# Optimization experiments

Measured on AMD Instinct MI355X. Metric: run time of the kernel, lower is better.

The kernel has to match this reference:

```python
import jax, jax.numpy as jnp
import numpy as np

B, L, V, E = 8, 2000, 50000, 300      # batch, doc len, vocab, embed dim
NL, LW = 8922, 10                     # num labels, words per label desc
F_, K, H = 200, 10, 200               # num_filters, kernel_size, label_hidden
FEAT = E + H                          # feat_size = 500


def setup_inputs():
    key = jax.random.key(0)
    ks = jax.random.split(key, 12)
    n = lambda k, sh, s=0.02: jax.random.normal(k, sh, jnp.float32) * s
    x = jax.random.randint(ks[0], (B, L), 0, V)
    y = (jax.random.uniform(ks[1], (B, NL)) < 0.01).astype(jnp.float32)
    mask = jnp.ones((B, L), jnp.float32)
    word_emb = n(ks[2], (V, E), 0.1)
    label_idx_matrix = jax.random.randint(ks[3], (NL, LW), 0, V)
    label_idx_mask = jnp.ones((NL, LW), jnp.float32)
    adj_matrix = (jax.random.uniform(ks[4], (NL, NL)) < 0.002).astype(jnp.float32)
    num_neighbors = jnp.maximum(adj_matrix.sum(axis=1), 1.0)
    return {
        'x': x, 'y': y, 'mask': mask,
        'word_emb': word_emb,
        'label_idx_matrix': label_idx_matrix,
        'label_idx_mask': label_idx_mask,
        'adj_matrix': adj_matrix,
        'num_neighbors': num_neighbors,
        'Wg': n(ks[5], (E, H)), 'bg': jnp.zeros((H,), jnp.float32),
        'Wc': n(ks[6], (F_, E, K)), 'bc': jnp.zeros((F_,), jnp.float32),
        'Wp': n(ks[7], (F_, E)), 'bp': jnp.zeros((E,), jnp.float32),
        'Wo': n(ks[8], (F_, FEAT)), 'bo': jnp.zeros((FEAT,), jnp.float32),
    }


def reference(x, y, mask, word_emb, label_idx_matrix, label_idx_mask,
              adj_matrix, num_neighbors, Wg, bg, Wc, bc, Wp, bp, Wo, bo):
    # --- average label embedding over label description words ---
    le = word_emb[label_idx_matrix]                              # [NL, LW, E]
    avg = (le * label_idx_mask[..., None]).sum(1)
    avg = avg / label_idx_mask.sum(axis=-1, keepdims=True)       # [NL, E]
    # --- conv graph encoder over label hierarchy ---
    agg = (adj_matrix @ avg) / num_neighbors[:, None]            # [NL, E]
    gh = jax.nn.relu(agg @ Wg + bg)                              # [NL, H]
    graph_emb = jnp.concatenate([avg, gh], axis=-1)              # [NL, FEAT]
    # --- document encoding (dropouts are identity in eval) ---
    xe = word_emb[x] * mask[..., None]                           # [B, L, E]
    c = jax.lax.conv_general_dilated(
        xe.transpose(0, 2, 1), Wc, window_strides=(1,), padding='VALID',
        dimension_numbers=('NCH', 'OIH', 'NCH')) + bc[None, :, None]
    c = jax.nn.relu(c).transpose(0, 2, 1)                        # [B, Lp, F]
    pj = jnp.tanh(c @ Wp + bp)                                   # [B, Lp, E]
    # --- label-wise attention ---
    scores = jnp.einsum('ble,ne->bnl', pj, avg)                  # [B, NL, Lp]
    attn = jax.nn.softmax(scores, axis=-1)
    attn_out = jnp.einsum('bnl,blf->bnf', attn, c)               # [B, NL, F]
    proj = jax.nn.relu(attn_out @ Wo + bo)                       # [B, NL, FEAT]
    logits = (graph_emb[None] * proj).sum(-1)                    # [B, NL]
    # --- BCE-with-logits (sum) / batch ---
    bce = jnp.maximum(logits, 0.0) - logits * y + jnp.log1p(jnp.exp(-jnp.abs(logits)))
    loss = bce.sum() / B
    return (logits, loss)
```

## Files before the change

kernel.cpp:

```cpp
#include <hip/hip_runtime.h>
#include <math.h>

#define B_    8
#define L_    2000
#define V_    50000
#define E_    300
#define NL_   8922
#define NLP_  8960
#define LW_   10
#define F_    200
#define KW_   10
#define H_    200
#define FEAT_ 500
#define LP_   1991

typedef __attribute__((ext_vector_type(8))) short bf16x8;
typedef __attribute__((ext_vector_type(4))) float f32x4;

static __device__ __forceinline__ unsigned short f2b(float f) {
  unsigned u = __builtin_bit_cast(unsigned, f);
  u += 0x7FFF + ((u >> 16) & 1);
  return (unsigned short)(u >> 16);
}
static __device__ __forceinline__ float b2f(unsigned short u) {
  unsigned v = ((unsigned)u) << 16;
  return __builtin_bit_cast(float, v);
}
static __device__ __forceinline__ float fast_tanh(float x) {
  x = fminf(fmaxf(x, -10.f), 10.f);
  float t = __expf(2.f * x);
  return (t - 1.f) / (t + 1.f);
}
static __device__ __forceinline__ void stage16(const void* g, void* l) {
  __builtin_amdgcn_global_load_lds(
      (const __attribute__((address_space(1))) unsigned int*)g,
      (__attribute__((address_space(3))) unsigned int*)l, 16, 0, 0);
}

#define MFMA(a, b, c) __builtin_amdgcn_mfma_f32_16x16x32_bf16(a, b, c, 0, 0, 0)


__global__ __launch_bounds__(256) void k_avg(const float* __restrict__ we,
                                             const int* __restrict__ lidx,
                                             const float* __restrict__ lmask,
                                             float* __restrict__ avg,
                                             unsigned short* __restrict__ avgb,
                                             unsigned short* __restrict__ geF) {
  int idx = blockIdx.x * 256 + threadIdx.x;
  if (idx >= NLP_ * 80) return;
  int n = idx / 80, e4 = idx - n * 80;
  if (n >= NL_ || e4 >= 75) {
    *(ushort4*)&avgb[(size_t)n * 320 + e4 * 4] = make_ushort4(0, 0, 0, 0);
    return;
  }
  float ax = 0.f, ay = 0.f, az = 0.f, aw = 0.f, ms = 0.f;
#pragma unroll
  for (int w = 0; w < LW_; ++w) {
    float mw = lmask[n * LW_ + w];
    const float4 f = *(const float4*)&we[(size_t)lidx[n * LW_ + w] * E_ + e4 * 4];
    ax = fmaf(f.x, mw, ax); ay = fmaf(f.y, mw, ay);
    az = fmaf(f.z, mw, az); aw = fmaf(f.w, mw, aw);
    ms += mw;
  }
  float inv = 1.f / ms;
  float4 v = {ax * inv, ay * inv, az * inv, aw * inv};
  *(float4*)&avg[(size_t)n * 300 + e4 * 4] = v;
  *(ushort4*)&avgb[(size_t)n * 320 + e4 * 4] =
      make_ushort4(f2b(v.x), f2b(v.y), f2b(v.z), f2b(v.w));
  int ntg = n >> 4, quad = (n >> 2) & 3, r = n & 3;
  int ftg = (e4 * 4) >> 4, c0 = (e4 * 4) & 15;
  size_t tb = (((size_t)ntg * 32 + ftg) << 8);
  float vv[4] = {v.x, v.y, v.z, v.w};
#pragma unroll
  for (int t = 0; t < 4; ++t)
    geF[(tb + quad * 16 + c0 + t) * 4 + r] = f2b(vv[t]);
}

__global__ __launch_bounds__(256) void k_agg(const float* __restrict__ adj,
                                             const float* __restrict__ avg,
                                             const float* __restrict__ nnb,
                                             unsigned short* __restrict__ aggF) {
  __shared__ int s_idx[1024];
  __shared__ float s_val[1024];
  __shared__ float s_agg[320];
  __shared__ int s_cnt;
  const int n = blockIdx.x;
  const int tid = threadIdx.x;
  if (tid == 0) s_cnt = 0;
  __syncthreads();
  const float* row = adj + (size_t)n * NL_;
  for (int j = tid; j < NL_; j += 256) {
    float v = row[j];
    if (v != 0.f) {
      int p = atomicAdd(&s_cnt, 1);
      if (p < 1024) { s_idx[p] = j; s_val[p] = v; }
    }
  }
  __syncthreads();
  const int m = min(s_cnt, 1024);
  const float inv = 1.f / nnb[n];
  float a0 = 0.f, a1 = 0.f;
  for (int i = 0; i < m; ++i) {
    const float* ar = avg + (size_t)s_idx[i] * 300;
    float v = s_val[i];
    a0 = fmaf(v, ar[tid], a0);
    if (tid < E_ - 256) a1 = fmaf(v, ar[tid + 256], a1);
  }
  s_agg[tid] = a0 * inv;
  if (tid < E_ - 256) s_agg[tid + 256] = a1 * inv;
  if (tid >= 44 && tid < 64) s_agg[tid + 256] = 0.f;
  __syncthreads();
  if (tid < 320) {
    int e = tid;
    int ks = e >> 5, qA = (e >> 3) & 3, jj = e & 7;
    aggF[(((size_t)((n >> 4) * 10 + ks)) << 9) + ((qA << 4) + (n & 15)) * 8 + jj] =
        f2b(s_agg[e]);
  }
}

__global__ __launch_bounds__(256) void k_gh2(const unsigned short* __restrict__ aggF,
                                             const unsigned short* __restrict__ WgF,
                                             const float* __restrict__ bg,
                                             unsigned short* __restrict__ geF) {
  const int n0g = blockIdx.x * 64;
  const int tid = threadIdx.x;
  const int wv = tid >> 6, lane = tid & 63, quad = lane >> 4, c16 = lane & 15;
  const int mt = wv;
  f32x4 acc[14];
#pragma unroll
  for (int nt = 0; nt < 14; ++nt) acc[nt] = (f32x4){0.f, 0.f, 0.f, 0.f};
#pragma unroll
  for (int ks = 0; ks < 10; ++ks) {
    bf16x8 a = *(const bf16x8*)
        &aggF[(((size_t)(((n0g >> 4) + mt) * 10 + ks)) << 9) + (lane << 3)];
#pragma unroll
    for (int nt = 0; nt < 14; ++nt) {
      bf16x8 bw = *(const bf16x8*)&WgF[(((size_t)(nt * 10 + ks)) << 9) + (lane << 3)];
      acc[nt] = MFMA(a, bw, acc[nt]);
    }
  }
#pragma unroll
  for (int nt = 0; nt < 14; ++nt) {
    int h = nt * 16 + c16;
    if (h < H_) {
      float bgv = bg[h];
      int feat = 300 + h;
      int ftg = feat >> 4, cg = feat & 15;
#pragma unroll
      for (int r = 0; r < 4; ++r) {
        int n = n0g + mt * 16 + quad * 4 + r;
        if (n < NL_)
          geF[((((size_t)(n >> 4) * 32 + ftg) << 8) + (quad << 4) + cg) * 4 + r] =
              f2b(fmaxf(acc[nt][r] + bgv, 0.f));
      }
    }
  }
}

__global__ __launch_bounds__(256) void k_wprep(const float* __restrict__ Wc,
                                               const float* __restrict__ Wp,
                                               const float* __restrict__ Wo,
                                               const float* __restrict__ Wg,
                                               unsigned short* __restrict__ WcF,
                                               unsigned short* __restrict__ WpF,
                                               unsigned short* __restrict__ WoF,
                                               unsigned short* __restrict__ WgF) {
  int idx = blockIdx.x * 256 + threadIdx.x;
  if (idx < 819200) {
    int koff = idx / (16 * 10 * 512);
    int rem = idx - koff * (16 * 10 * 512);
    int ft = rem / (10 * 512);
    int rem2 = rem - ft * (10 * 512);
    int ks = rem2 >> 9, t = rem2 & 511;
    int lane = t >> 3, j = t & 7;
    int f = ft * 16 + (lane & 15);
    int e = ks * 32 + (lane >> 4) * 8 + j;
    float v = (f < F_ && e < E_) ? Wc[((size_t)f * E_ + e) * KW_ + koff] : 0.f;
    WcF[idx] = f2b(v);
    return;
  }
  idx -= 819200;
  if (idx < 71680) {
    int et = idx / (7 * 512);
    int rem = idx - et * (7 * 512);
    int kt = rem >> 9, t = rem & 511;
    int lane = t >> 3, j = t & 7;
    int e = et * 16 + (lane & 15);
    int f = kt * 32 + (lane >> 4) * 8 + j;
    float v = (e < E_ && f < F_) ? Wp[(size_t)f * E_ + e] : 0.f;
    WpF[idx] = f2b(v);
    return;
  }
  idx -= 71680;
  if (idx < 114688) {
    int g = idx / (7 * 512);
    int rem = idx - g * (7 * 512);
    int kt = rem >> 9, t = rem & 511;
    int lane = t >> 3, j = t & 7;
    int feat = g * 16 + (lane & 15);
    int f = kt * 32 + (lane >> 4) * 8 + j;
    float v = (feat < FEAT_ && f < F_) ? Wo[(size_t)f * FEAT_ + feat] : 0.f;
    WoF[idx] = f2b(v);
    return;
  }
  idx -= 114688;
  if (idx < 71680) {
    int nt = idx / (10 * 512);
    int rem = idx - nt * (10 * 512);
    int ks = rem >> 9, t = rem & 511;
    int lane = t >> 3, j = t & 7;
    int h = nt * 16 + (lane & 15);
    int e = ks * 32 + (lane >> 4) * 8 + j;
    float v = (h < H_ && e < E_) ? Wg[(size_t)e * H_ + h] : 0.f;
    WgF[idx] = f2b(v);
  }
}

__global__ __launch_bounds__(256) void k_cpj(const int* __restrict__ x,
                                             const float* __restrict__ mask,
                                             const float* __restrict__ we,
                                             const unsigned short* __restrict__ WcF,
                                             const float* __restrict__ bc,
                                             const unsigned short* __restrict__ WpF,
                                             const float* __restrict__ bp,
                                             unsigned short* __restrict__ cF,
                                             unsigned short* __restrict__ pjF) {
  __shared__ __attribute__((aligned(16))) unsigned char smem[78896];
  unsigned short* s_xe  = (unsigned short*)smem;
  unsigned short* s_pjF = (unsigned short*)smem;
  unsigned short* s_cA  = (unsigned short*)(smem + 50224);

  const int b = blockIdx.y;
  const int l0 = blockIdx.x * 64;
  const int tid = threadIdx.x;
  const int wv = tid >> 6, lane = tid & 63, quad = lane >> 4, c16 = lane & 15;

  for (int i = tid; i < 73 * 75; i += 256) {
    int row = i / 75, e4 = i - row * 75;
    int l = l0 + row;
    float4 v = {0.f, 0.f, 0.f, 0.f};
    if (l < L_) {
      int bl = b * L_ + l;
      v = *(const float4*)&we[(size_t)x[bl] * E_ + e4 * 4];
      float mm = mask[bl];
      v.x *= mm; v.y *= mm; v.z *= mm; v.w *= mm;
    }
    *(ushort4*)&s_xe[row * 344 + e4 * 4] =
        make_ushort4(f2b(v.x), f2b(v.y), f2b(v.z), f2b(v.w));
  }
  for (int i = tid; i < 73 * 5; i += 256) {
    int row = i / 5, c = i - row * 5;
    *(ushort4*)&s_xe[row * 344 + (75 + c) * 4] = make_ushort4(0, 0, 0, 0);
  }
  __syncthreads();

  f32x4 acc[4][4];
#pragma unroll
  for (int mt = 0; mt < 4; ++mt)
#pragma unroll
    for (int j = 0; j < 4; ++j) acc[mt][j] = (f32x4){0.f, 0.f, 0.f, 0.f};
  for (int koff = 0; koff < KW_; ++koff) {
#pragma unroll
    for (int ks = 0; ks < 10; ++ks) {
      bf16x8 a[4];
#pragma unroll
      for (int mt = 0; mt < 4; ++mt)
        a[mt] = *(const bf16x8*)&s_xe[(mt * 16 + c16 + koff) * 344 + ks * 32 + quad * 8];
#pragma unroll
      for (int jj = 0; jj < 4; ++jj) {
        bf16x8 bw = *(const bf16x8*)
            &WcF[(((size_t)((koff * 16 + wv * 4 + jj) * 10 + ks)) << 9) + (lane << 3)];
#pragma unroll
        for (int mt = 0; mt < 4; ++mt) acc[mt][jj] = MFMA(a[mt], bw, acc[mt][jj]);
      }
    }
  }
  unsigned short* cFb = cF + (size_t)b * (16 * 64 * 512);
#pragma unroll
  for (int jj = 0; jj < 4; ++jj) {
    const int ft2 = wv * 4 + jj;
    const int f = ft2 * 16 + c16;
    const float bcv = (f < F_) ? bc[f] : 0.f;
    const int kt = ft2 >> 1;
    const int qA = ((ft2 & 1) << 1) | (c16 >> 3);
    const int jA = c16 & 7;
#pragma unroll
    for (int mt = 0; mt < 4; ++mt) {
      unsigned short u[4];
#pragma unroll
      for (int r = 0; r < 4; ++r) u[r] = f2b(fmaxf(acc[mt][jj][r] + bcv, 0.f));
      int su = (l0 >> 5) + (mt >> 1);
      int lane_c = ((((mt & 1) << 1) | (quad >> 1)) << 4) + c16;
      *(ushort4*)&cFb[(((size_t)(ft2 * 64 + su)) << 9) + lane_c * 8 + ((quad & 1) << 2)] =
          make_ushort4(u[0], u[1], u[2], u[3]);
      if (ft2 < 14) {
#pragma unroll
        for (int r = 0; r < 4; ++r)
          s_cA[(((size_t)(mt * 7 + kt)) << 9) + ((qA << 4) + quad * 4 + r) * 8 + jA] = u[r];
      }
    }
  }
  __syncthreads();

  f32x4 pacc[4][5];
#pragma unroll
  for (int mt = 0; mt < 4; ++mt)
#pragma unroll
    for (int j = 0; j < 5; ++j) pacc[mt][j] = (f32x4){0.f, 0.f, 0.f, 0.f};
#pragma unroll
  for (int kt = 0; kt < 7; ++kt) {
    bf16x8 a[4];
#pragma unroll
    for (int mt = 0; mt < 4; ++mt)
      a[mt] = *(const bf16x8*)&s_cA[(((size_t)(mt * 7 + kt)) << 9) + (lane << 3)];
#pragma unroll
    for (int j = 0; j < 5; ++j) {
      bf16x8 bw = *(const bf16x8*)
          &WpF[(((size_t)((wv * 5 + j) * 7 + kt)) << 9) + (lane << 3)];
#pragma unroll
      for (int mt = 0; mt < 4; ++mt) pacc[mt][j] = MFMA(a[mt], bw, pacc[mt][j]);
    }
  }
  __syncthreads();
#pragma unroll
  for (int j = 0; j < 5; ++j) {
    const int et = wv * 5 + j;
    const int e = et * 16 + c16;
    const float bpe = (e < E_) ? bp[e] : 0.f;
    const int ks = et >> 1;
    const int qP = ((et & 1) << 1) | (c16 >> 3);
    const int jP = c16 & 7;
#pragma unroll
    for (int mt = 0; mt < 4; ++mt) {
#pragma unroll
      for (int r = 0; r < 4; ++r) {
        float v = (e < E_) ? fast_tanh(pacc[mt][j][r] + bpe) : 0.f;
        s_pjF[(((size_t)(mt * 10 + ks)) << 9) + ((qP << 4) + quad * 4 + r) * 8 + jP] = f2b(v);
      }
    }
  }
  __syncthreads();
  {
    unsigned short* dst = pjF + (((size_t)((b * 128 + (l0 >> 4)) * 10)) << 9);
    for (int i = tid; i < 2560; i += 256)
      *(uint4*)&dst[i * 8] = *(const uint4*)&s_pjF[i * 8];
  }
}

__global__ __launch_bounds__(256, 2) void k_attn(
    const unsigned short* __restrict__ pjF,
    const unsigned short* __restrict__ cF,
    const unsigned short* __restrict__ avgb,
    const unsigned short* __restrict__ WoF,
    const unsigned short* __restrict__ geF,
    const float* __restrict__ bo,
    float* __restrict__ out) {
  __shared__ __attribute__((aligned(16))) unsigned char smem[74752];
  unsigned short* Ps  = (unsigned short*)(smem + 69632);
  float* s_wsum = (float*)(smem + 73728);
  float* s_sum  = (float*)(smem + 74240);
  float* s_lg   = (float*)(smem + 74496);
  unsigned short* AOs = (unsigned short*)smem;

  const int tid = threadIdx.x;
  const int b  = blockIdx.x & 7;
  const int n0 = (blockIdx.x >> 3) << 6;
  const int wv = tid >> 6, lane = tid & 63, quad = lane >> 4, c16 = lane & 15;
  const int lh = wv & 1, nh = wv >> 1;

  if (tid < 64) s_lg[tid] = 0.f;

  bf16x8 bavg[10][2];
#pragma unroll
  for (int ks = 0; ks < 10; ++ks)
#pragma unroll
    for (int nt = 0; nt < 2; ++nt)
      bavg[ks][nt] = *(const bf16x8*)
          &avgb[(size_t)(n0 + nh * 32 + nt * 16 + c16) * 320 + ks * 32 + quad * 8];

  const unsigned short* pjb = pjF + (size_t)b * (128 * 10 * 512);
  const unsigned short* cFb = cF + (size_t)b * (16 * 64 * 512);

  {
    const unsigned char* pg = (const unsigned char*)pjb;
#pragma unroll
    for (int t = 0; t < 5; ++t) {
      int off = (wv * 5 + t) << 10;
      stage16(pg + off + lane * 16, smem + off);
    }
#pragma unroll
    for (int t = 0; t < 4; ++t) {
      int ft = wv + t * 4;
      if (ft < 14)
        stage16((const unsigned char*)cFb + (((size_t)(ft * 64)) << 10) + lane * 16,
                smem + 20480 + (ft << 10));
    }
  }

  f32x4 o[2][7];
#pragma unroll
  for (int nt = 0; nt < 2; ++nt)
#pragma unroll
    for (int j = 0; j < 7; ++j) o[nt][j] = (f32x4){0.f, 0.f, 0.f, 0.f};
  float ssum[2] = {0.f, 0.f};

  for (int lc = 0; lc < 64; ++lc) {
    __builtin_amdgcn_s_waitcnt(0);
    __syncthreads();
    unsigned char* cur = smem + ((lc & 1) ? 34816 : 0);
    unsigned char* nxt = smem + ((lc & 1) ? 0 : 34816);
    if (lc + 1 < 64) {
      const unsigned char* pg =
          (const unsigned char*)pjb + (((size_t)((lc + 1) * 20)) << 10);
#pragma unroll
      for (int t = 0; t < 5; ++t) {
        int off = (wv * 5 + t) << 10;
        stage16(pg + off + lane * 16, nxt + off);
      }
#pragma unroll
      for (int t = 0; t < 4; ++t) {
        int ft = wv + t * 4;
        if (ft < 14)
          stage16((const unsigned char*)cFb + (((size_t)(ft * 64 + lc + 1)) << 10) + lane * 16,
                  nxt + 20480 + (ft << 10));
      }
    }
    const unsigned short* pt = (const unsigned short*)cur;
    f32x4 acc0 = (f32x4){0.f, 0.f, 0.f, 0.f};
    f32x4 acc1 = (f32x4){0.f, 0.f, 0.f, 0.f};
#pragma unroll
    for (int ks = 0; ks < 10; ++ks) {
      bf16x8 a = *(const bf16x8*)(pt + ((lh * 10 + ks) << 9) + (lane << 3));
      acc0 = MFMA(a, bavg[ks][0], acc0);
      acc1 = MFMA(a, bavg[ks][1], acc1);
    }
    const int lb = (lc << 5) + lh * 16 + quad * 4;
#pragma unroll
    for (int nt = 0; nt < 2; ++nt) {
      f32x4 av = nt ? acc1 : acc0;
      float psum = 0.f;
      unsigned short u[4];
#pragma unroll
      for (int r = 0; r < 4; ++r) {
        float p = __expf(av[r]);
        if (lc >= 62 && (lb + r >= LP_)) p = 0.f;
        psum += p;
        u[r] = f2b(p);
      }
      *(ushort4*)&Ps[((nh * 2 + nt) << 9) +
                     ((lh * 2 + (quad >> 1)) * 16 + c16) * 8 + ((quad & 1) << 2)] =
          make_ushort4(u[0], u[1], u[2], u[3]);
      psum += __shfl_xor(psum, 16);
      psum += __shfl_xor(psum, 32);
      ssum[nt] += psum;
    }
    __syncthreads();
    {
      bf16x8 aP0 = *(const bf16x8*)&Ps[((nh * 2) << 9) + (lane << 3)];
      bf16x8 aP1 = *(const bf16x8*)&Ps[((nh * 2 + 1) << 9) + (lane << 3)];
      const unsigned short* cc = (const unsigned short*)(cur + 20480);
#pragma unroll
      for (int ft = 0; ft < 7; ++ft) {
        bf16x8 bC = *(const bf16x8*)(cc + ((lh * 7 + ft) << 9) + (lane << 3));
        o[0][ft] = MFMA(aP0, bC, o[0][ft]);
        o[1][ft] = MFMA(aP1, bC, o[1][ft]);
      }
    }
  }

  if (lane < 16) {
    s_wsum[wv * 32 + lane] = ssum[0];
    s_wsum[wv * 32 + 16 + lane] = ssum[1];
  }
  __syncthreads();
  if (tid < 64) {
    int g = tid >> 5, idx = tid & 31;
    s_sum[tid] = s_wsum[(g * 2) * 32 + idx] + s_wsum[(g * 2 + 1) * 32 + idx];
  }
  __syncthreads();
#pragma unroll
  for (int nt = 0; nt < 2; ++nt) {
    const int ntile = nh * 2 + nt;
    float inv4[4];
#pragma unroll
    for (int r = 0; r < 4; ++r) inv4[r] = 1.f / s_sum[ntile * 16 + quad * 4 + r];
#pragma unroll
    for (int ft = 0; ft < 7; ++ft) {
      int f = (lh * 7 + ft) * 16 + c16;
      int kt = f >> 5, qA = (f >> 3) & 3, jA = f & 7;
#pragma unroll
      for (int r = 0; r < 4; ++r)
        AOs[((ntile * 7 + kt) << 9) + ((qA << 4) + quad * 4 + r) * 8 + jA] =
            f2b(o[nt][ft][r] * inv4[r]);
    }
  }
  __syncthreads();
  float la[4][4];
#pragma unroll
  for (int nt = 0; nt < 4; ++nt)
#pragma unroll
    for (int r = 0; r < 4; ++r) la[nt][r] = 0.f;
#pragma unroll
  for (int i = 0; i < 8; ++i) {
    const int ftg = wv * 8 + i;
    const int feat = (ftg << 4) + c16;
    f32x4 pa[4];
#pragma unroll
    for (int nt = 0; nt < 4; ++nt) pa[nt] = (f32x4){0.f, 0.f, 0.f, 0.f};
    const unsigned short* wof = WoF + (((size_t)(ftg * 7)) << 9) + (lane << 3);
#pragma unroll
    for (int kt = 0; kt < 7; ++kt) {
      bf16x8 bw = *(const bf16x8*)(wof + (kt << 9));
#pragma unroll
      for (int nt = 0; nt < 4; ++nt) {
        bf16x8 aa = *(const bf16x8*)&AOs[((nt * 7 + kt) << 9) + (lane << 3)];
        pa[nt] = MFMA(aa, bw, pa[nt]);
      }
    }
    const float bof = (feat < FEAT_) ? bo[feat] : 0.f;
#pragma unroll
    for (int nt = 0; nt < 4; ++nt) {
      ushort4 g4 = *(const ushort4*)
          &geF[((((size_t)(n0 >> 4) + nt) * 32 + ftg) << 8) + (lane << 2)];
      float gv[4] = {b2f(g4.x), b2f(g4.y), b2f(g4.z), b2f(g4.w)};
#pragma unroll
      for (int r = 0; r < 4; ++r) {
        float pv = fmaxf(pa[nt][r] + bof, 0.f);
        la[nt][r] = fmaf(pv, gv[r], la[nt][r]);
      }
    }
  }
#pragma unroll
  for (int nt = 0; nt < 4; ++nt)
#pragma unroll
    for (int r = 0; r < 4; ++r) {
      float v = la[nt][r];
      v += __shfl_xor(v, 1); v += __shfl_xor(v, 2);
      v += __shfl_xor(v, 4); v += __shfl_xor(v, 8);
      if (c16 == 0) atomicAdd(&s_lg[nt * 16 + quad * 4 + r], v);
    }
  __syncthreads();
  if (tid < 64) {
    int ng = n0 + tid;
    if (ng < NL_) out[(size_t)b * NL_ + ng] = s_lg[tid];
  }
}

__global__ __launch_bounds__(1024) void k_loss(const float* __restrict__ lgts,
                                               const float* __restrict__ y,
                                               float* __restrict__ loss) {
  __shared__ float red[1024];
  const int tid = threadIdx.x;
  float s = 0.f;
  for (int i = tid; i < B_ * NL_; i += 1024) {
    float l = lgts[i], yy = y[i];
    s += fmaxf(l, 0.f) - l * yy + log1pf(expf(-fabsf(l)));
  }
  red[tid] = s;
  __syncthreads();
  for (int st = 512; st > 0; st >>= 1) {
    if (tid < st) red[tid] += red[tid + st];
    __syncthreads();
  }
  if (tid == 0) loss[0] = red[0] * (1.f / B_);
}

extern "C" void kernel_launch(void* const* d_in, const int* in_sizes, int n_in,
                              void* d_out, int out_size, void* d_ws, size_t ws_size,
                              hipStream_t stream) {
  const int*   x     = (const int*)  d_in[0];
  const float* y     = (const float*)d_in[1];
  const float* mask  = (const float*)d_in[2];
  const float* we    = (const float*)d_in[3];
  const int*   lidx  = (const int*)  d_in[4];
  const float* lmask = (const float*)d_in[5];
  const float* adj   = (const float*)d_in[6];
  const float* nnb   = (const float*)d_in[7];
  const float* Wg    = (const float*)d_in[8];
  const float* bg    = (const float*)d_in[9];
  const float* Wc    = (const float*)d_in[10];
  const float* bc    = (const float*)d_in[11];
  const float* Wp    = (const float*)d_in[12];
  const float* bp    = (const float*)d_in[13];
  const float* Wo    = (const float*)d_in[14];
  const float* bo    = (const float*)d_in[15];
  float* out = (float*)d_out;
  char* W = (char*)d_ws;

  unsigned short* pjF  = (unsigned short*)(W + 0);
  unsigned short* cF   = (unsigned short*)(W + 10485760);
  unsigned short* avgb = (unsigned short*)(W + 18874368);
  unsigned short* geF  = (unsigned short*)(W + 24608768);
  unsigned short* aggF = (unsigned short*)(W + 33783808);
  unsigned short* WcF  = (unsigned short*)(W + 44490208);
  unsigned short* WpF  = (unsigned short*)(W + 46128608);
  unsigned short* WoF  = (unsigned short*)(W + 46271968);
  unsigned short* WgF  = (unsigned short*)(W + 46501344);
  float*          avg  = (float*)(W + 0);

  hipMemsetAsync(geF, 0, 9175040, stream);
  k_wprep<<<(819200 + 71680 + 114688 + 71680 + 255) / 256, 256, 0, stream>>>(
      Wc, Wp, Wo, Wg, WcF, WpF, WoF, WgF);
  k_avg<<<(NLP_ * 80 + 255) / 256, 256, 0, stream>>>(we, lidx, lmask, avg, avgb, geF);
  k_agg<<<NL_, 256, 0, stream>>>(adj, avg, nnb, aggF);
  k_gh2<<<140, 256, 0, stream>>>(aggF, WgF, bg, geF);
  k_cpj<<<dim3(32, B_), 256, 0, stream>>>(x, mask, we, WcF, bc, WpF, bp, cF, pjF);
  k_attn<<<140 * 8, 256, 0, stream>>>(pjF, cF, avgb, WoF, geF, bo, out);
  k_loss<<<1, 1024, 0, stream>>>(out, y, out + B_ * NL_);
}
```

Baseline: 1.034 ms.

## Software-pipeline attention loop and drop mid-iteration barrier; vectorize adjacency scan

The attention kernel is restructured so each chunk's P·C MFMA runs one iteration late, using double-buffered P tiles and C tiles. This removes the second __syncthreads per chunk and lets the score MFMAs and exp work overlap with the previous chunk's output MFMAs, at the cost of more LDS and an epilogue step. The bf16 rounding of P now truncates, and the softmax sum is taken from the truncated values so numerator and denominator stay consistent. The adjacency row scan in k_agg also reads float2 instead of scalar floats.

```diff
diff --git a/kernel.cpp b/kernel.cpp
--- a/kernel.cpp
+++ b/kernel.cpp
@@ -22,6 +22,9 @@
   u += 0x7FFF + ((u >> 16) & 1);
   return (unsigned short)(u >> 16);
 }
+static __device__ __forceinline__ unsigned short f2b_t(float f) {
+  return (unsigned short)(__builtin_bit_cast(unsigned, f) >> 16);
+}
 static __device__ __forceinline__ float b2f(unsigned short u) {
   unsigned v = ((unsigned)u) << 16;
   return __builtin_bit_cast(float, v);
@@ -88,12 +91,16 @@
   const int tid = threadIdx.x;
   if (tid == 0) s_cnt = 0;
   __syncthreads();
-  const float* row = adj + (size_t)n * NL_;
-  for (int j = tid; j < NL_; j += 256) {
-    float v = row[j];
-    if (v != 0.f) {
+  const float2* row2 = (const float2*)(adj + (size_t)n * NL_);
+  for (int j = tid; j < NL_ / 2; j += 256) {
+    float2 v = row2[j];
+    if (v.x != 0.f) {
       int p = atomicAdd(&s_cnt, 1);
-      if (p < 1024) { s_idx[p] = j; s_val[p] = v; }
+      if (p < 1024) { s_idx[p] = 2 * j; s_val[p] = v.x; }
+    }
+    if (v.y != 0.f) {
+      int p = atomicAdd(&s_cnt, 1);
+      if (p < 1024) { s_idx[p] = 2 * j + 1; s_val[p] = v.y; }
     }
   }
   __syncthreads();
@@ -355,11 +362,11 @@
     const unsigned short* __restrict__ geF,
     const float* __restrict__ bo,
     float* __restrict__ out) {
-  __shared__ __attribute__((aligned(16))) unsigned char smem[74752];
+  __shared__ __attribute__((aligned(16))) unsigned char smem[78848];
   unsigned short* Ps  = (unsigned short*)(smem + 69632);
-  float* s_wsum = (float*)(smem + 73728);
-  float* s_sum  = (float*)(smem + 74240);
-  float* s_lg   = (float*)(smem + 74496);
+  float* s_wsum = (float*)(smem + 77824);
+  float* s_sum  = (float*)(smem + 78336);
+  float* s_lg   = (float*)(smem + 78592);
   unsigned short* AOs = (unsigned short*)smem;
 
   const int tid = threadIdx.x;
@@ -388,83 +395,92 @@
       int off = (wv * 5 + t) << 10;
       stage16(pg + off + lane * 16, smem + off);
     }
+  }
+
+  f32x4 o[2][7];
+#pragma unroll
+  for (int nt = 0; nt < 2; ++nt)
+#pragma unroll
+    for (int j = 0; j < 7; ++j) o[nt][j] = (f32x4){0.f, 0.f, 0.f, 0.f};
+  float ssum[2] = {0.f, 0.f};
+
+  for (int c = 0; c < 64; ++c) {
+    __builtin_amdgcn_s_waitcnt(0);
+    __syncthreads();
+    const int cb = c & 1;
+    const unsigned short* pjcur = (const unsigned short*)(smem + cb * 20480);
+    const unsigned short* cfprev = (const unsigned short*)(smem + 40960 + (cb ^ 1) * 14336);
+    if (c + 1 < 64) {
+      const unsigned char* pg =
+          (const unsigned char*)pjb + (((size_t)((c + 1) * 20)) << 10);
+#pragma unroll
+      for (int t = 0; t < 5; ++t) {
+        int off = (wv * 5 + t) << 10;
+        stage16(pg + off + lane * 16, smem + (cb ^ 1) * 20480 + off);
+      }
+    }
 #pragma unroll
     for (int t = 0; t < 4; ++t) {
       int ft = wv + t * 4;
       if (ft < 14)
-        stage16((const unsigned char*)cFb + (((size_t)(ft * 64)) << 10) + lane * 16,
-                smem + 20480 + (ft << 10));
-    }
-  }
-
-  f32x4 o[2][7];
-#pragma unroll
-  for (int nt = 0; nt < 2; ++nt)
-#pragma unroll
-    for (int j = 0; j < 7; ++j) o[nt][j] = (f32x4){0.f, 0.f, 0.f, 0.f};
-  float ssum[2] = {0.f, 0.f};
-
-  for (int lc = 0; lc < 64; ++lc) {
-    __builtin_amdgcn_s_waitcnt(0);
-    __syncthreads();
-    unsigned char* cur = smem + ((lc & 1) ? 34816 : 0);
-    unsigned char* nxt = smem + ((lc & 1) ? 0 : 34816);
-    if (lc + 1 < 64) {
-      const unsigned char* pg =
-          (const unsigned char*)pjb + (((size_t)((lc + 1) * 20)) << 10);
-#pragma unroll
-      for (int t = 0; t < 5; ++t) {
-        int off = (wv * 5 + t) << 10;
-        stage16(pg + off + lane * 16, nxt + off);
-      }
-#pragma unroll
-      for (int t = 0; t < 4; ++t) {
-        int ft = wv + t * 4;
-        if (ft < 14)
-          stage16((const unsigned char*)cFb + (((size_t)(ft * 64 + lc + 1)) << 10) + lane * 16,
-                  nxt + 20480 + (ft << 10));
-      }
-    }
-    const unsigned short* pt = (const unsigned short*)cur;
+        stage16((const unsigned char*)cFb + (((size_t)(ft * 64 + c)) << 10) + lane * 16,
+                smem + 40960 + cb * 14336 + (ft << 10));
+    }
     f32x4 acc0 = (f32x4){0.f, 0.f, 0.f, 0.f};
     f32x4 acc1 = (f32x4){0.f, 0.f, 0.f, 0.f};
 #pragma unroll
     for (int ks = 0; ks < 10; ++ks) {
-      bf16x8 a = *(const bf16x8*)(pt + ((lh * 10 + ks) << 9) + (lane << 3));
+      bf16x8 a = *(const bf16x8*)(pjcur + ((lh * 10 + ks) << 9) + (lane << 3));
       acc0 = MFMA(a, bavg[ks][0], acc0);
       acc1 = MFMA(a, bavg[ks][1], acc1);
     }
-    const int lb = (lc << 5) + lh * 16 + quad * 4;
-#pragma unroll
-    for (int nt = 0; nt < 2; ++nt) {
-      f32x4 av = nt ? acc1 : acc0;
-      float psum = 0.f;
-      unsigned short u[4];
-#pragma unroll
-      for (int r = 0; r < 4; ++r) {
-        float p = __expf(av[r]);
-        if (lc >= 62 && (lb + r >= LP_)) p = 0.f;
-        psum += p;
-        u[r] = f2b(p);
-      }
-      *(ushort4*)&Ps[((nh * 2 + nt) << 9) +
-                     ((lh * 2 + (quad >> 1)) * 16 + c16) * 8 + ((quad & 1) << 2)] =
-          make_ushort4(u[0], u[1], u[2], u[3]);
-      psum += __shfl_xor(psum, 16);
-      psum += __shfl_xor(psum, 32);
-      ssum[nt] += psum;
-    }
-    __syncthreads();
-    {
-      bf16x8 aP0 = *(const bf16x8*)&Ps[((nh * 2) << 9) + (lane << 3)];
-      bf16x8 aP1 = *(const bf16x8*)&Ps[((nh * 2 + 1) << 9) + (lane << 3)];
-      const unsigned short* cc = (const unsigned short*)(cur + 20480);
+    if (c) {
+      const unsigned short* Pp = Ps + ((cb ^ 1) << 11);
+      bf16x8 aP0 = *(const bf16x8*)(Pp + ((nh * 2) << 9) + (lane << 3));
+      bf16x8 aP1 = *(const bf16x8*)(Pp + ((nh * 2 + 1) << 9) + (lane << 3));
 #pragma unroll
       for (int ft = 0; ft < 7; ++ft) {
-        bf16x8 bC = *(const bf16x8*)(cc + ((lh * 7 + ft) << 9) + (lane << 3));
+        bf16x8 bC = *(const bf16x8*)(cfprev + ((lh * 7 + ft) << 9) + (lane << 3));
         o[0][ft] = MFMA(aP0, bC, o[0][ft]);
         o[1][ft] = MFMA(aP1, bC, o[1][ft]);
       }
+    }
+    {
+      unsigned short* Pc = Ps + (cb << 11);
+      const int lb = (c << 5) + lh * 16 + quad * 4;
+#pragma unroll
+      for (int nt = 0; nt < 2; ++nt) {
+        f32x4 av = nt ? acc1 : acc0;
+        float psum = 0.f;
+        unsigned short u[4];
+#pragma unroll
+        for (int r = 0; r < 4; ++r) {
+          float p = __expf(av[r]);
+          if (c >= 62 && (lb + r >= LP_)) p = 0.f;
+          u[r] = f2b_t(p);
+          psum += b2f(u[r]);
+        }
+        *(ushort4*)&Pc[((nh * 2 + nt) << 9) +
+                       ((lh * 2 + (quad >> 1)) * 16 + c16) * 8 + ((quad & 1) << 2)] =
+            make_ushort4(u[0], u[1], u[2], u[3]);
+        psum += __shfl_xor(psum, 16);
+        psum += __shfl_xor(psum, 32);
+        ssum[nt] += psum;
+      }
+    }
+  }
+  __builtin_amdgcn_s_waitcnt(0);
+  __syncthreads();
+  {
+    const unsigned short* cfprev = (const unsigned short*)(smem + 40960 + 14336);
+    const unsigned short* Pp = Ps + (1 << 11);
+    bf16x8 aP0 = *(const bf16x8*)(Pp + ((nh * 2) << 9) + (lane << 3));
+    bf16x8 aP1 = *(const bf16x8*)(Pp + ((nh * 2 + 1) << 9) + (lane << 3));
+#pragma unroll
+    for (int ft = 0; ft < 7; ++ft) {
+      bf16x8 bC = *(const bf16x8*)(cfprev + ((lh * 7 + ft) << 9) + (lane << 3));
+      o[0][ft] = MFMA(aP0, bC, o[0][ft]);
+      o[1][ft] = MFMA(aP1, bC, o[1][ft]);
     }
   }
 
```

New measurement: 992.6 us. 1.04x faster.
